# Optimization experiments

Measured on AMD Instinct MI355X. Metric: run time of the kernel, lower is better.

The kernel has to match this reference:

```python
import jax, jax.numpy as jnp
import numpy as np

H = 16          # nhead
N_LAYERS = 4    # stacks (weights are SHARED across stacks, as in the torch module)
PAD_IDX = 1
EPS = 1e-6
NEG = -1e9


def _pos_encoding(S, d):
    den = jnp.exp(-jnp.arange(0, d, 2, dtype=jnp.float32) * (np.log(10000.0) / d))
    ang = jnp.arange(S, dtype=jnp.float32)[:, None] * den[None, :]  # (S, d/2)
    pe = jnp.zeros((S, d), jnp.float32)
    pe = pe.at[:, 0::2].set(jnp.sin(ang)).at[:, 1::2].set(jnp.cos(ang))
    return pe


def _layer_norm(x, g, b):
    mu = jnp.mean(x, axis=-1, keepdims=True)
    var = jnp.mean((x - mu) ** 2, axis=-1, keepdims=True)
    return (x - mu) * jax.lax.rsqrt(var + EPS) * g + b


def _split_heads(x):
    B, S, d = x.shape
    return x.reshape(B, S, H, d // H).transpose(0, 2, 1, 3)  # (B,H,S,dk)


def _mha(q_in, k_in, v_in, mask, wq, bq, wk, bk, wv, bv, wo, bo):
    q = _split_heads(q_in @ wq + bq)
    k = _split_heads(k_in @ wk + bk)
    v = _split_heads(v_in @ wv + bv)
    dk = v.shape[-1]
    score = jnp.einsum('bhqd,bhkd->bhqk', q, k) / jnp.sqrt(jnp.float32(dk))
    if mask is not None:
        score = jnp.where(mask, score, NEG)
    p = jax.nn.softmax(score, axis=-1)
    out = jnp.einsum('bhqk,bhkd->bhqd', p, v)
    B, _, S, _ = out.shape
    out = out.transpose(0, 2, 1, 3).reshape(B, S, H * dk)
    return out @ wo + bo


def setup_inputs() -> dict:
    key = jax.random.key(0)
    B, St, Sm, d, dff, V = 4, 1024, 1024, 1024, 4096, 32000
    ks = jax.random.split(key, 32)
    sc = 1.0 / np.sqrt(d)
    inp = {
        'target_result': jax.random.randint(ks[0], (B, St), 0, V),
        'memory': jax.random.normal(ks[1], (B, Sm, d), jnp.float32),
        'emb': jax.random.normal(ks[2], (V, d), jnp.float32) * sc,
        'ff_w1': jax.random.normal(ks[3], (d, dff), jnp.float32) * sc,
        'ff_b1': jnp.zeros((dff,), jnp.float32),
        'ff_w2': jax.random.normal(ks[4], (dff, d), jnp.float32) / np.sqrt(dff),
        'ff_b2': jnp.zeros((d,), jnp.float32),
        'ln_g': jnp.ones((d,), jnp.float32),
        'ln_b': jnp.zeros((d,), jnp.float32),
    }
    i = 5
    for pre in ('sa', 'xa'):
        for nm in ('q', 'k', 'v', 'o'):
            inp[f'{pre}_w{nm}'] = jax.random.normal(ks[i], (d, d), jnp.float32) * sc
            inp[f'{pre}_b{nm}'] = jnp.zeros((d,), jnp.float32)
            i += 1
    return inp


def reference(target_result, memory, emb,
              sa_wq, sa_bq, sa_wk, sa_bk, sa_wv, sa_bv, sa_wo, sa_bo,
              xa_wq, xa_bq, xa_wk, xa_bk, xa_wv, xa_bv, xa_wo, xa_bo,
              ff_w1, ff_b1, ff_w2, ff_b2, ln_g, ln_b):
    B, St = target_result.shape
    d = emb.shape[1]
    # embed + scale + positional encoding (dropout = eval/identity)
    x = emb[target_result] * jnp.sqrt(jnp.float32(d)) + _pos_encoding(St, d)[None]
    # masks: pad mask (B,1,St,1) & causal (St,St) -> (B,1,St,St); source mask all-ones -> None
    pad = (target_result != PAD_IDX)[:, None, :, None]
    causal = jnp.tril(jnp.ones((St, St), bool))[None, None]
    tgt_mask = pad & causal
    out = x
    for _ in range(N_LAYERS):
        n = _layer_norm(out, ln_g, ln_b)
        out = out + _mha(n, n, n, tgt_mask,
                         sa_wq, sa_bq, sa_wk, sa_bk, sa_wv, sa_bv, sa_wo, sa_bo)
        n = _layer_norm(out, ln_g, ln_b)
        out = out + _mha(n, memory, memory, None,
                         xa_wq, xa_bq, xa_wk, xa_bk, xa_wv, xa_bv, xa_wo, xa_bo)
        n = _layer_norm(out, ln_g, ln_b)
        out = out + (jax.nn.relu(n @ ff_w1 + ff_b1) @ ff_w2 + ff_b2)
    return _layer_norm(out, ln_g, ln_b)
```

## Files before the change

### kernel.cpp

```cpp
#include <hip/hip_runtime.h>

typedef unsigned short u16;
typedef unsigned int u32;
typedef float f32x4 __attribute__((ext_vector_type(4)));
typedef float f32x16 __attribute__((ext_vector_type(16)));
typedef __bf16 bf16x8 __attribute__((ext_vector_type(8)));
typedef short short8 __attribute__((ext_vector_type(8)));
typedef u32 u32x4 __attribute__((ext_vector_type(4)));

#define DINLINE static __device__ __forceinline__

DINLINE u16 f2bf(float f) {
  u32 u = __builtin_bit_cast(u32, f);
  u += 0x7fffu + ((u >> 16) & 1u);
  return (u16)(u >> 16);
}

DINLINE f32x4 mfma16(short8 a, short8 b, f32x4 c) {
  return __builtin_amdgcn_mfma_f32_16x16x32_bf16(
      __builtin_bit_cast(bf16x8, a), __builtin_bit_cast(bf16x8, b), c, 0, 0, 0);
}

DINLINE f32x16 mfma32(short8 a, short8 b, f32x16 c) {
  return __builtin_amdgcn_mfma_f32_32x32x16_bf16(
      __builtin_bit_cast(bf16x8, a), __builtin_bit_cast(bf16x8, b), c, 0, 0, 0);
}

DINLINE u32 cvtpk(float lo, float hi) {
  u32 r;
  asm("v_cvt_pk_bf16_f32 %0, %1, %2" : "=v"(r) : "v"(lo), "v"(hi));
  return r;
}

DINLINE void plswap(u32& a, u32& b) {
  auto r = __builtin_amdgcn_permlane32_swap(a, b, false, false);
  a = (u32)r[0];
  b = (u32)r[1];
}

DINLINE void gld16(const void* g, void* l) {
  __builtin_amdgcn_global_load_lds(
      (const __attribute__((address_space(1))) void*)g,
      (__attribute__((address_space(3))) void*)l, 16, 0, 0);
}

__global__ __launch_bounds__(256) void transpose_wt(const float* __restrict__ src,
                                                    u16* __restrict__ dst, int K, int N,
                                                    float scale) {
  __shared__ float tile[32][33];
  int n0 = blockIdx.x * 32, k0 = blockIdx.y * 32;
  int tx = threadIdx.x, ty = threadIdx.y;
#pragma unroll
  for (int j = 0; j < 32; j += 8)
    tile[ty + j][tx] = src[(size_t)(k0 + ty + j) * N + n0 + tx];
  __syncthreads();
#pragma unroll
  for (int j = 0; j < 32; j += 8)
    dst[(size_t)(n0 + ty + j) * K + k0 + tx] = f2bf(tile[tx][ty + j] * scale);
}

__global__ __launch_bounds__(256) void cvt_bf16(const float* __restrict__ src,
                                                u16* __restrict__ dst) {
  size_t i = (size_t)blockIdx.x * 256 + threadIdx.x;
  float4 v = ((const float4*)src)[i];
  u32 lo = (u32)f2bf(v.x) | ((u32)f2bf(v.y) << 16);
  u32 hi = (u32)f2bf(v.z) | ((u32)f2bf(v.w) << 16);
  uint2 o; o.x = lo; o.y = hi;
  ((uint2*)dst)[i] = o;
}

__global__ void concat3(const float* __restrict__ a, const float* __restrict__ b,
                        const float* __restrict__ c, float* __restrict__ o, float sa) {
  int i = blockIdx.x * 256 + threadIdx.x;
  float v = (i < 1024) ? a[i] * sa : (i < 2048 ? b[i - 1024] : c[i - 2048]);
  o[i] = v;
}

__global__ void scale_vec(const float* __restrict__ a, float* __restrict__ o, float s) {
  int i = blockIdx.x * 256 + threadIdx.x;
  o[i] = a[i] * s;
}

__global__ __launch_bounds__(256) void pe_k(float* __restrict__ pe) {
  int s = blockIdx.x;
  for (int c = threadIdx.x; c < 1024; c += 256) {
    int i = c >> 1;
    float den = expf(-(float)(2 * i) * 0.0089944739960705f);
    float ang = (float)s * den;
    pe[s * 1024 + c] = (c & 1) ? cosf(ang) : sinf(ang);
  }
}

__global__ __launch_bounds__(256) void embed_pe(const int* __restrict__ tgt,
                                                const float* __restrict__ emb,
                                                const float* __restrict__ pe,
                                                float* __restrict__ x) {
  int row = blockIdx.x;
  int s = row & 1023;
  int tok = tgt[row];
  float4 e = ((const float4*)(emb + (size_t)tok * 1024))[threadIdx.x];
  float4 p = ((const float4*)(pe + (size_t)s * 1024))[threadIdx.x];
  float4 o;
  o.x = e.x * 32.0f + p.x; o.y = e.y * 32.0f + p.y;
  o.z = e.z * 32.0f + p.z; o.w = e.w * 32.0f + p.w;
  ((float4*)(x + (size_t)row * 1024))[threadIdx.x] = o;
}

template <int MODE>
__global__ __launch_bounds__(256) void ln_k(const float* __restrict__ X,
                                            const float* __restrict__ g,
                                            const float* __restrict__ bta,
                                            u16* __restrict__ obf,
                                            float* __restrict__ of) {
  int row = blockIdx.x;
  int t = threadIdx.x;
  float4 v = ((const float4*)(X + (size_t)row * 1024))[t];
  float s = v.x + v.y + v.z + v.w;
  float sq = v.x * v.x + v.y * v.y + v.z * v.z + v.w * v.w;
#pragma unroll
  for (int o = 1; o < 64; o <<= 1) {
    s += __shfl_xor(s, o);
    sq += __shfl_xor(sq, o);
  }
  __shared__ float red[8];
  int wid = t >> 6;
  if ((t & 63) == 0) { red[wid * 2] = s; red[wid * 2 + 1] = sq; }
  __syncthreads();
  s = red[0] + red[2] + red[4] + red[6];
  sq = red[1] + red[3] + red[5] + red[7];
  float mean = s * (1.0f / 1024.0f);
  float var = sq * (1.0f / 1024.0f) - mean * mean;
  float rstd = rsqrtf(var + 1e-6f);
  float4 gv = ((const float4*)g)[t];
  float4 bv = ((const float4*)bta)[t];
  float y0 = (v.x - mean) * rstd * gv.x + bv.x;
  float y1 = (v.y - mean) * rstd * gv.y + bv.y;
  float y2 = (v.z - mean) * rstd * gv.z + bv.z;
  float y3 = (v.w - mean) * rstd * gv.w + bv.w;
  if (MODE == 1) {
    float4 o4; o4.x = y0; o4.y = y1; o4.z = y2; o4.w = y3;
    ((float4*)of)[(size_t)row * 256 + t] = o4;
  } else {
    u32 lo = (u32)f2bf(y0) | ((u32)f2bf(y1) << 16);
    u32 hi = (u32)f2bf(y2) | ((u32)f2bf(y3) << 16);
    uint2 o2; o2.x = lo; o2.y = hi;
    ((uint2*)obf)[(size_t)row * 256 + t] = o2;
  }
}

__global__ __launch_bounds__(256) void vtrans(const u16* __restrict__ V, int sV,
                                              u16* __restrict__ Vt) {
  __shared__ u16 tile[32][33];
  int s0 = blockIdx.x * 32, d0 = blockIdx.y * 32, bh = blockIdx.z;
  int b = bh >> 4, h = bh & 15;
  const u16* src = V + (size_t)b * 1024 * sV + h * 64;
  int tx = threadIdx.x, ty = threadIdx.y;
#pragma unroll
  for (int j = 0; j < 32; j += 8)
    tile[ty + j][tx] = src[(size_t)(s0 + ty + j) * sV + d0 + tx];
  __syncthreads();
  u16* dst = Vt + (size_t)bh * 64 * 1024;
#pragma unroll
  for (int j = 0; j < 32; j += 8)
    dst[(size_t)(d0 + ty + j) * 1024 + s0 + tx] = tile[tx][ty + j];
}

template <int BM, int EPI>
__global__ __launch_bounds__(256) void gemm2(
    const u16* __restrict__ A, const u16* __restrict__ Bt,
    const float* __restrict__ bias, float* __restrict__ X,
    u16* __restrict__ Cbf, int N, int K) {
  constexpr int ABYT = BM * 128;
  constexpr int BBYT = 128 * 128;
  constexpr int MF = BM / 32;
  __shared__ __align__(16) char smem[2 * (ABYT + BBYT)];

  const int tid = threadIdx.x;
  const int w = tid >> 6, l = tid & 63;
  const int lg = l >> 4, lc = l & 15;
  const int m0 = blockIdx.y * BM, n0 = blockIdx.x * 128;
  const int wr = w >> 1, wc = w & 1;
  const char* Ab = (const char*)A;
  const char* Bb = (const char*)Bt;
  const size_t sA = (size_t)K * 2;

  f32x4 acc[MF][4];
  const f32x4 zv = {0.f, 0.f, 0.f, 0.f};
#pragma unroll
  for (int m = 0; m < MF; ++m)
#pragma unroll
    for (int n = 0; n < 4; ++n) acc[m][n] = zv;

  const int srow = l >> 3;
  const int scol = ((l & 7) ^ srow) << 4;

  auto stage = [&](char* bufA, char* bufB, int kt) {
    const size_t kb = (size_t)kt << 7;
#pragma unroll
    for (int i = 0; i < BM / 32; ++i) {
      const int r = i * 32 + w * 8 + srow;
      gld16(Ab + (size_t)(m0 + r) * sA + kb + scol, bufA + (i * 4 + w) * 1024 + l * 16);
    }
#pragma unroll
    for (int i = 0; i < 4; ++i) {
      const int r = i * 32 + w * 8 + srow;
      gld16(Bb + (size_t)(n0 + r) * sA + kb + scol, bufB + (i * 4 + w) * 1024 + l * 16);
    }
  };

  stage(smem, smem + ABYT, 0);
  __syncthreads();

  const int nkt = K >> 6;
  int cur = 0;
  for (int kt = 0; kt < nkt; ++kt) {
    char* As = smem + cur * (ABYT + BBYT);
    char* Bs = As + ABYT;
    if (kt + 1 < nkt) {
      char* An = smem + (cur ^ 1) * (ABYT + BBYT);
      stage(An, An + ABYT, kt + 1);
    }
#pragma unroll
    for (int ks = 0; ks < 2; ++ks) {
      short8 af[MF], bf4[4];
#pragma unroll
      for (int m = 0; m < MF; ++m) {
        int row = wr * (BM / 2) + m * 16 + lc;
        int col = (ks * 64 + (lg << 4)) ^ ((row & 7) << 4);
        af[m] = *(const short8*)(As + row * 128 + col);
      }
#pragma unroll
      for (int n = 0; n < 4; ++n) {
        int row = wc * 64 + n * 16 + lc;
        int col = (ks * 64 + (lg << 4)) ^ ((row & 7) << 4);
        bf4[n] = *(const short8*)(Bs + row * 128 + col);
      }
#pragma unroll
      for (int m = 0; m < MF; ++m)
#pragma unroll
        for (int n = 0; n < 4; ++n) acc[m][n] = mfma16(af[m], bf4[n], acc[m][n]);
    }
    __syncthreads();
    cur ^= 1;
  }

  float bv[4];
#pragma unroll
  for (int n = 0; n < 4; ++n) bv[n] = bias[n0 + wc * 64 + n * 16 + lc];

  if (EPI <= 1) {
    u16* ct = (u16*)smem;
#pragma unroll
    for (int m = 0; m < MF; ++m)
#pragma unroll
      for (int n = 0; n < 4; ++n)
#pragma unroll
        for (int r = 0; r < 4; ++r) {
          int row = wr * (BM / 2) + m * 16 + (lg << 2) + r;
          int col = wc * 64 + n * 16 + lc;
          float v = acc[m][n][r] + bv[n];
          if (EPI == 1) v = v > 0.f ? v : 0.f;
          ct[row * 136 + col] = f2bf(v);
        }
    __syncthreads();
#pragma unroll
    for (int j = 0; j < BM / 16; ++j) {
      int c = j * 256 + tid;
      int row = c >> 4, colb = (c & 15) * 8;
      *(short8*)(Cbf + (size_t)(m0 + row) * N + n0 + colb) =
          *(const short8*)(ct + row * 136 + colb);
    }
  } else {
    float* cf = (float*)smem;
#pragma unroll
    for (int m = 0; m < MF; ++m)
#pragma unroll
      for (int n = 0; n < 4; ++n)
#pragma unroll
        for (int r = 0; r < 4; ++r) {
          int row = wr * (BM / 2) + m * 16 + (lg << 2) + r;
          int col = wc * 64 + n * 16 + lc;
          cf[row * 128 + col] = acc[m][n][r] + bv[n];
        }
    __syncthreads();
#pragma unroll
    for (int j = 0; j < BM / 8; ++j) {
      int c = j * 256 + tid;
      int row = c >> 5, colb = (c & 31) * 4;
      size_t idx = (size_t)(m0 + row) * N + n0 + colb;
      float4 s = *(const float4*)(cf + row * 128 + colb);
      float4 xv = *(const float4*)(X + idx);
      xv.x += s.x; xv.y += s.y; xv.z += s.z; xv.w += s.w;
      *(float4*)(X + idx) = xv;
    }
  }
}

template <bool CAUSAL>
__global__ __launch_bounds__(256) void attn_lds(
    const u16* __restrict__ Qp, int sQ, const u16* __restrict__ Kp, int sK,
    const u16* __restrict__ Vt, const int* __restrict__ tgt,
    u16* __restrict__ Out) {
  __shared__ __align__(16) char smem[2][16384];
  const int tid = threadIdx.x;
  const int w = tid >> 6, l = tid & 63;
  const int bh = blockIdx.x & 63, sub = blockIdx.x >> 6;
  const int b = bh >> 4, h = bh & 15;
  const int lq = l & 31, hi = l >> 5;
  const int qt = sub * 4 + w;
  const int q0 = qt * 32;

  const char* Kc = (const char*)(Kp + (size_t)b * 1024 * sK + h * 64);
  const char* Vc = (const char*)(Vt + (size_t)bh * 64 * 1024);
  const u16* Qh = Qp + (size_t)b * 1024 * sQ + h * 64;

  short8 qb[4];
  {
    const u16* qrow = Qh + (size_t)(q0 + lq) * sQ + hi * 8;
#pragma unroll
    for (int c = 0; c < 4; ++c) qb[c] = *(const short8*)(qrow + c * 16);
  }

  bool row_ok = true;
  int my_nkt = 16;
  int blk_nkt = CAUSAL ? (sub * 2 + 2) : 16;
  if (CAUSAL) {
    row_ok = (tgt[b * 1024 + q0 + lq] != 1);
    bool anypad_w = __any(!row_ok);
    __shared__ int s_pad;
    if (tid == 0) s_pad = 0;
    __syncthreads();
    if (anypad_w && l == 0) s_pad = 1;
    __syncthreads();
    if (s_pad) { my_nkt = 16; blk_nkt = 16; }
    else my_nkt = (qt >> 1) + 1;
  }

  const int srow = l >> 3;
  const int scol = ((l & 7) ^ srow) << 4;
  auto stage = [&](int buf, int kt) {
    const int k0 = kt * 64;
    char* Ks = smem[buf];
    char* Vs = smem[buf] + 8192;
#pragma unroll
    for (int i = 0; i < 2; ++i) {
      const int r = i * 32 + w * 8 + srow;
      gld16(Kc + (size_t)(k0 + r) * sK * 2 + scol, Ks + r * 128);
      gld16(Vc + (size_t)r * 2048 + (size_t)k0 * 2 + scol, Vs + r * 128);
    }
  };

  float m = -3.0e38f, lsum = 0.f;
  f32x16 oacc[2];
#pragma unroll
  for (int r = 0; r < 16; ++r) { oacc[0][r] = 0.f; oacc[1][r] = 0.f; }

  stage(0, 0);
  __syncthreads();
  int cur = 0;

  for (int kt = 0; kt < blk_nkt; ++kt) {
    if (kt + 1 < blk_nkt) stage(cur ^ 1, kt + 1);
    if (kt < my_nkt) {
      const char* Ks = smem[cur];
      const char* Vs = smem[cur] + 8192;
      const int k0 = kt * 64;
      f32x16 st[2];
#pragma unroll
      for (int s = 0; s < 2; ++s) {
        const int row = s * 32 + lq;
        const int swz = (row & 7) << 4;
        f32x16 a;
#pragma unroll
        for (int r = 0; r < 16; ++r) a[r] = 0.f;
#pragma unroll
        for (int c = 0; c < 4; ++c) {
          short8 kb = *(const short8*)(Ks + row * 128 + ((c * 32 + hi * 16) ^ swz));
          a = mfma32(kb, qb[c], a);
        }
        st[s] = a;
      }
      if (CAUSAL) {
#pragma unroll
        for (int s = 0; s < 2; ++s) {
          if (!row_ok || (k0 + s * 32 + 31 > q0)) {
#pragma unroll
            for (int r = 0; r < 16; ++r) {
              int kg = k0 + s * 32 + (r & 3) + 8 * (r >> 2) + 4 * hi;
              bool ok = row_ok && (kg <= q0 + lq);
              if (!ok) st[s][r] = -1e9f;
            }
          }
        }
      }
      float tm;
      {
        float v[16];
#pragma unroll
        for (int r = 0; r < 16; ++r) v[r] = fmaxf(st[0][r], st[1][r]);
#pragma unroll
        for (int w2 = 8; w2 >= 1; w2 >>= 1)
#pragma unroll
          for (int r = 0; r < w2; ++r) v[r] = fmaxf(v[r], v[r + w2]);
        tm = v[0];
      }
      tm = fmaxf(tm, __shfl_xor(tm, 32));
      if (!__all(tm <= m + 8.0f)) {
        float mn = fmaxf(m, tm);
        float alpha = __expf(m - mn);
        lsum *= alpha;
        m = mn;
#pragma unroll
        for (int r = 0; r < 16; ++r) {
          int crow = (r & 3) + 8 * (r >> 2) + 4 * hi;
          float av = __shfl(alpha, crow);
          oacc[0][r] *= av;
          oacc[1][r] *= av;
        }
      }
      float tsa0 = 0.f, tsa1 = 0.f, tsa2 = 0.f, tsa3 = 0.f;
#pragma unroll
      for (int s = 0; s < 2; ++s) {
#pragma unroll
        for (int r = 0; r < 16; ++r) {
          float e = __expf(st[s][r] - m);
          st[s][r] = e;
          if ((r & 3) == 0) tsa0 += e;
          else if ((r & 3) == 1) tsa1 += e;
          else if ((r & 3) == 2) tsa2 += e;
          else tsa3 += e;
        }
      }
      float ts = (tsa0 + tsa1) + (tsa2 + tsa3);
      ts += __shfl_xor(ts, 32);
      lsum += ts;
      short8 pa[4];
#pragma unroll
      for (int s = 0; s < 2; ++s) {
        u32 cc[8];
#pragma unroll
        for (int t = 0; t < 4; ++t) {
          cc[2 * t]     = cvtpk(st[s][4 * t + 0], st[s][4 * t + 1]);
          cc[2 * t + 1] = cvtpk(st[s][4 * t + 2], st[s][4 * t + 3]);
        }
        plswap(cc[0], cc[2]);
        plswap(cc[1], cc[3]);
        plswap(cc[4], cc[6]);
        plswap(cc[5], cc[7]);
        u32x4 w0 = {cc[0], cc[1], cc[2], cc[3]};
        u32x4 w1 = {cc[4], cc[5], cc[6], cc[7]};
        pa[2 * s]     = __builtin_bit_cast(short8, w0);
        pa[2 * s + 1] = __builtin_bit_cast(short8, w1);
      }
#pragma unroll
      for (int dt = 0; dt < 2; ++dt) {
        const int row = dt * 32 + lq;
        const int swz = (row & 7) << 4;
#pragma unroll
        for (int c = 0; c < 4; ++c) {
          short8 vb = *(const short8*)(Vs + row * 128 + ((c * 32 + hi * 16) ^ swz));
          oacc[dt] = mfma32(pa[c], vb, oacc[dt]);
        }
      }
    }
    __syncthreads();
    cur ^= 1;
  }

#pragma unroll
  for (int r = 0; r < 16; ++r) {
    int crow = (r & 3) + 8 * (r >> 2) + 4 * hi;
    float lv = __shfl(lsum, crow);
    float linv = 1.0f / lv;
    int qg = q0 + crow;
    size_t base = ((size_t)b * 1024 + qg) * 1024 + h * 64 + lq;
    Out[base] = f2bf(oacc[0][r] * linv);
    Out[base + 32] = f2bf(oacc[1][r] * linv);
  }
}

extern "C" void kernel_launch(void* const* d_in, const int* in_sizes, int n_in,
                              void* d_out, int out_size, void* d_ws, size_t ws_size,
                              hipStream_t stream) {
  const int* tgt = (const int*)d_in[0];
  const float* memory = (const float*)d_in[1];
  const float* emb = (const float*)d_in[2];
  const float* ff_w1 = (const float*)d_in[3];
  const float* ff_b1 = (const float*)d_in[4];
  const float* ff_w2 = (const float*)d_in[5];
  const float* ff_b2 = (const float*)d_in[6];
  const float* ln_g = (const float*)d_in[7];
  const float* ln_b = (const float*)d_in[8];
  const float* sa_wq = (const float*)d_in[9];
  const float* sa_bq = (const float*)d_in[10];
  const float* sa_wk = (const float*)d_in[11];
  const float* sa_bk = (const float*)d_in[12];
  const float* sa_wv = (const float*)d_in[13];
  const float* sa_bv = (const float*)d_in[14];
  const float* sa_wo = (const float*)d_in[15];
  const float* sa_bo = (const float*)d_in[16];
  const float* xa_wq = (const float*)d_in[17];
  const float* xa_bq = (const float*)d_in[18];
  const float* xa_wk = (const float*)d_in[19];
  const float* xa_bk = (const float*)d_in[20];
  const float* xa_wv = (const float*)d_in[21];
  const float* xa_bv = (const float*)d_in[22];
  const float* xa_wo = (const float*)d_in[23];
  const float* xa_bo = (const float*)d_in[24];

  char* ws = (char*)d_ws;
  size_t off = 0;
  auto alloc = [&](size_t bytes) {
    char* p = ws + off;
    off += (bytes + 255) & ~(size_t)255;
    return p;
  };
  float* x   = (float*)alloc(4096ull * 1024 * 4);
  u16* nbf   = (u16*)alloc(4096ull * 1024 * 2);
  u16* qkv   = (u16*)alloc(4096ull * 3072 * 2);
  u16* q2    = (u16*)alloc(4096ull * 1024 * 2);
  u16* attn  = (u16*)alloc(4096ull * 1024 * 2);
  u16* vt    = (u16*)alloc(64ull * 64 * 1024 * 2);
  u16* kx    = (u16*)alloc(4096ull * 1024 * 2);
  u16* vtx   = (u16*)alloc(64ull * 64 * 1024 * 2);
  u16* h1    = (u16*)alloc(4096ull * 4096 * 2);
  u16* memb  = (u16*)alloc(4096ull * 1024 * 2);
  u16* w_qkv = (u16*)alloc(3072ull * 1024 * 2);
  u16* w_sao = (u16*)alloc(1024ull * 1024 * 2);
  u16* w_xaq = (u16*)alloc(1024ull * 1024 * 2);
  u16* w_xak = (u16*)alloc(1024ull * 1024 * 2);
  u16* w_xav = (u16*)alloc(1024ull * 1024 * 2);
  u16* w_xao = (u16*)alloc(1024ull * 1024 * 2);
  u16* w_ff1 = (u16*)alloc(4096ull * 1024 * 2);
  u16* w_ff2 = (u16*)alloc(1024ull * 4096 * 2);
  float* b_qkv = (float*)alloc(3072 * 4);
  float* b_xaq = (float*)alloc(1024 * 4);
  float* pe    = (float*)alloc(1024ull * 1024 * 4);

  dim3 blk(256);
  dim3 b32(32, 8);
  const float QS = 0.125f;

  transpose_wt<<<dim3(32, 32), b32, 0, stream>>>(sa_wq, w_qkv, 1024, 1024, QS);
  transpose_wt<<<dim3(32, 32), b32, 0, stream>>>(sa_wk, w_qkv + 1024 * 1024, 1024, 1024, 1.f);
  transpose_wt<<<dim3(32, 32), b32, 0, stream>>>(sa_wv, w_qkv + 2048 * 1024, 1024, 1024, 1.f);
  transpose_wt<<<dim3(32, 32), b32, 0, stream>>>(sa_wo, w_sao, 1024, 1024, 1.f);
  transpose_wt<<<dim3(32, 32), b32, 0, stream>>>(xa_wq, w_xaq, 1024, 1024, QS);
  transpose_wt<<<dim3(32, 32), b32, 0, stream>>>(xa_wk, w_xak, 1024, 1024, 1.f);
  transpose_wt<<<dim3(32, 32), b32, 0, stream>>>(xa_wv, w_xav, 1024, 1024, 1.f);
  transpose_wt<<<dim3(32, 32), b32, 0, stream>>>(xa_wo, w_xao, 1024, 1024, 1.f);
  transpose_wt<<<dim3(128, 32), b32, 0, stream>>>(ff_w1, w_ff1, 1024, 4096, 1.f);
  transpose_wt<<<dim3(32, 128), b32, 0, stream>>>(ff_w2, w_ff2, 4096, 1024, 1.f);
  concat3<<<12, blk, 0, stream>>>(sa_bq, sa_bk, sa_bv, b_qkv, QS);
  scale_vec<<<4, blk, 0, stream>>>(xa_bq, b_xaq, QS);
  cvt_bf16<<<4096, blk, 0, stream>>>(memory, memb);
  pe_k<<<1024, blk, 0, stream>>>(pe);
  embed_pe<<<4096, blk, 0, stream>>>(tgt, emb, pe, x);

  gemm2<64, 0><<<dim3(8, 64), blk, 0, stream>>>(memb, w_xak, xa_bk, nullptr, kx, 1024, 1024);
  gemm2<64, 0><<<dim3(8, 64), blk, 0, stream>>>(memb, w_xav, xa_bv, nullptr, attn, 1024, 1024);
  vtrans<<<dim3(32, 2, 64), b32, 0, stream>>>(attn, 1024, vtx);

  for (int layer = 0; layer < 4; ++layer) {
    ln_k<0><<<4096, blk, 0, stream>>>(x, ln_g, ln_b, nbf, nullptr);
    gemm2<128, 0><<<dim3(24, 32), blk, 0, stream>>>(nbf, w_qkv, b_qkv, nullptr, qkv, 3072, 1024);
    vtrans<<<dim3(32, 2, 64), b32, 0, stream>>>(qkv + 2048, 3072, vt);
    attn_lds<true><<<512, blk, 0, stream>>>(qkv, 3072, qkv + 1024, 3072, vt, tgt, attn);
    gemm2<64, 2><<<dim3(8, 64), blk, 0, stream>>>(attn, w_sao, sa_bo, x, nullptr, 1024, 1024);
    ln_k<0><<<4096, blk, 0, stream>>>(x, ln_g, ln_b, nbf, nullptr);
    gemm2<64, 0><<<dim3(8, 64), blk, 0, stream>>>(nbf, w_xaq, b_xaq, nullptr, q2, 1024, 1024);
    attn_lds<false><<<512, blk, 0, stream>>>(q2, 1024, kx, 1024, vtx, nullptr, attn);
    gemm2<64, 2><<<dim3(8, 64), blk, 0, stream>>>(attn, w_xao, xa_bo, x, nullptr, 1024, 1024);
    ln_k<0><<<4096, blk, 0, stream>>>(x, ln_g, ln_b, nbf, nullptr);
    gemm2<128, 1><<<dim3(32, 32), blk, 0, stream>>>(nbf, w_ff1, ff_b1, nullptr, h1, 4096, 1024);
    gemm2<64, 2><<<dim3(8, 64), blk, 0, stream>>>(h1, w_ff2, ff_b2, x, nullptr, 1024, 4096);
  }
  ln_k<1><<<4096, blk, 0, stream>>>(x, ln_g, ln_b, nullptr, (float*)d_out);
}
```

Before: 1.142 ms.

## Fuse V transpose into GEMM epilogue, bf16 residual copy, bigger attention stages, setprio

Adds a GEMM epilogue that writes V directly in the transposed per-head layout, so the separate vtrans kernels and the 3072-wide QKV output go away. The residual adds now also write a bf16 copy of x, which intermediate LayerNorms read instead of fp32, halving their read bytes but computing their statistics on rounded values. The attention kernel stages 128 keys per buffer with doubled LDS, and s_setprio is raised around the MFMA sections in both the GEMM and attention kernels. Together these aim to cut launches and memory traffic, at the cost of slight precision loss and lower attention occupancy.

```diff
diff --git a/kernel.cpp b/kernel.cpp
--- a/kernel.cpp
+++ b/kernel.cpp
@@ -14,6 +14,11 @@
   u32 u = __builtin_bit_cast(u32, f);
   u += 0x7fffu + ((u >> 16) & 1u);
   return (u16)(u >> 16);
+}
+
+DINLINE float b2f(u32 lo16) {
+  u32 u = lo16 << 16;
+  return __builtin_bit_cast(float, u);
 }
 
 DINLINE f32x4 mfma16(short8 a, short8 b, f32x4 c) {
@@ -94,7 +99,8 @@
 __global__ __launch_bounds__(256) void embed_pe(const int* __restrict__ tgt,
                                                 const float* __restrict__ emb,
                                                 const float* __restrict__ pe,
-                                                float* __restrict__ x) {
+                                                float* __restrict__ x,
+                                                u16* __restrict__ xbf) {
   int row = blockIdx.x;
   int s = row & 1023;
   int tok = tgt[row];
@@ -104,19 +110,30 @@
   o.x = e.x * 32.0f + p.x; o.y = e.y * 32.0f + p.y;
   o.z = e.z * 32.0f + p.z; o.w = e.w * 32.0f + p.w;
   ((float4*)(x + (size_t)row * 1024))[threadIdx.x] = o;
+  ushort4 ob;
+  ob.x = f2bf(o.x); ob.y = f2bf(o.y); ob.z = f2bf(o.z); ob.w = f2bf(o.w);
+  ((ushort4*)(xbf + (size_t)row * 1024))[threadIdx.x] = ob;
 }
 
 template <int MODE>
-__global__ __launch_bounds__(256) void ln_k(const float* __restrict__ X,
+__global__ __launch_bounds__(256) void ln_k(const float* __restrict__ Xf,
+                                            const u16* __restrict__ Xb,
                                             const float* __restrict__ g,
                                             const float* __restrict__ bta,
                                             u16* __restrict__ obf,
                                             float* __restrict__ of) {
   int row = blockIdx.x;
   int t = threadIdx.x;
-  float4 v = ((const float4*)(X + (size_t)row * 1024))[t];
-  float s = v.x + v.y + v.z + v.w;
-  float sq = v.x * v.x + v.y * v.y + v.z * v.z + v.w * v.w;
+  float v0, v1, v2, v3;
+  if (MODE == 1) {
+    float4 v = ((const float4*)(Xf + (size_t)row * 1024))[t];
+    v0 = v.x; v1 = v.y; v2 = v.z; v3 = v.w;
+  } else {
+    uint2 p2 = ((const uint2*)(Xb + (size_t)row * 1024))[t];
+    v0 = b2f(p2.x); v1 = b2f(p2.x >> 16); v2 = b2f(p2.y); v3 = b2f(p2.y >> 16);
+  }
+  float s = v0 + v1 + v2 + v3;
+  float sq = v0 * v0 + v1 * v1 + v2 * v2 + v3 * v3;
 #pragma unroll
   for (int o = 1; o < 64; o <<= 1) {
     s += __shfl_xor(s, o);
@@ -133,10 +150,10 @@
   float rstd = rsqrtf(var + 1e-6f);
   float4 gv = ((const float4*)g)[t];
   float4 bv = ((const float4*)bta)[t];
-  float y0 = (v.x - mean) * rstd * gv.x + bv.x;
-  float y1 = (v.y - mean) * rstd * gv.y + bv.y;
-  float y2 = (v.z - mean) * rstd * gv.z + bv.z;
-  float y3 = (v.w - mean) * rstd * gv.w + bv.w;
+  float y0 = (v0 - mean) * rstd * gv.x + bv.x;
+  float y1 = (v1 - mean) * rstd * gv.y + bv.y;
+  float y2 = (v2 - mean) * rstd * gv.z + bv.z;
+  float y3 = (v3 - mean) * rstd * gv.w + bv.w;
   if (MODE == 1) {
     float4 o4; o4.x = y0; o4.y = y1; o4.z = y2; o4.w = y3;
     ((float4*)of)[(size_t)row * 256 + t] = o4;
@@ -146,23 +163,6 @@
     uint2 o2; o2.x = lo; o2.y = hi;
     ((uint2*)obf)[(size_t)row * 256 + t] = o2;
   }
-}
-
-__global__ __launch_bounds__(256) void vtrans(const u16* __restrict__ V, int sV,
-                                              u16* __restrict__ Vt) {
-  __shared__ u16 tile[32][33];
-  int s0 = blockIdx.x * 32, d0 = blockIdx.y * 32, bh = blockIdx.z;
-  int b = bh >> 4, h = bh & 15;
-  const u16* src = V + (size_t)b * 1024 * sV + h * 64;
-  int tx = threadIdx.x, ty = threadIdx.y;
-#pragma unroll
-  for (int j = 0; j < 32; j += 8)
-    tile[ty + j][tx] = src[(size_t)(s0 + ty + j) * sV + d0 + tx];
-  __syncthreads();
-  u16* dst = Vt + (size_t)bh * 64 * 1024;
-#pragma unroll
-  for (int j = 0; j < 32; j += 8)
-    dst[(size_t)(d0 + ty + j) * 1024 + s0 + tx] = tile[tx][ty + j];
 }
 
 template <int BM, int EPI>
@@ -220,6 +220,7 @@
       char* An = smem + (cur ^ 1) * (ABYT + BBYT);
       stage(An, An + ABYT, kt + 1);
     }
+    __builtin_amdgcn_s_setprio(1);
 #pragma unroll
     for (int ks = 0; ks < 2; ++ks) {
       short8 af[MF], bf4[4];
@@ -240,6 +241,7 @@
 #pragma unroll
         for (int n = 0; n < 4; ++n) acc[m][n] = mfma16(af[m], bf4[n], acc[m][n]);
     }
+    __builtin_amdgcn_s_setprio(0);
     __syncthreads();
     cur ^= 1;
   }
@@ -270,7 +272,7 @@
       *(short8*)(Cbf + (size_t)(m0 + row) * N + n0 + colb) =
           *(const short8*)(ct + row * 136 + colb);
     }
-  } else {
+  } else if (EPI == 2) {
     float* cf = (float*)smem;
 #pragma unroll
     for (int m = 0; m < MF; ++m)
@@ -288,10 +290,36 @@
       int c = j * 256 + tid;
       int row = c >> 5, colb = (c & 31) * 4;
       size_t idx = (size_t)(m0 + row) * N + n0 + colb;
-      float4 s = *(const float4*)(cf + row * 128 + colb);
+      float4 s4 = *(const float4*)(cf + row * 128 + colb);
       float4 xv = *(const float4*)(X + idx);
-      xv.x += s.x; xv.y += s.y; xv.z += s.z; xv.w += s.w;
+      xv.x += s4.x; xv.y += s4.y; xv.z += s4.z; xv.w += s4.w;
       *(float4*)(X + idx) = xv;
+      ushort4 ob;
+      ob.x = f2bf(xv.x); ob.y = f2bf(xv.y); ob.z = f2bf(xv.z); ob.w = f2bf(xv.w);
+      *(ushort4*)(Cbf + idx) = ob;
+    }
+  } else {
+    u16* ct = (u16*)smem;
+#pragma unroll
+    for (int m = 0; m < MF; ++m)
+#pragma unroll
+      for (int n = 0; n < 4; ++n)
+#pragma unroll
+        for (int r = 0; r < 4; ++r) {
+          int row = wr * (BM / 2) + m * 16 + (lg << 2) + r;
+          int col = wc * 64 + n * 16 + lc;
+          ct[col * 136 + row] = f2bf(acc[m][n][r] + bv[n]);
+        }
+    __syncthreads();
+    const int bb = m0 >> 10, ms = m0 & 1023;
+#pragma unroll
+    for (int j = 0; j < BM / 16; ++j) {
+      int flat = j * 256 + tid;
+      int sb = flat & (BM / 8 - 1);
+      int col = flat / (BM / 8);
+      int n = n0 + col;
+      u16* dst = Cbf + (size_t)(((bb << 4) + (n >> 6)) * 64 + (n & 63)) * 1024 + ms + sb * 8;
+      *(short8*)dst = *(const short8*)(ct + col * 136 + sb * 8);
     }
   }
 }
@@ -301,7 +329,7 @@
     const u16* __restrict__ Qp, int sQ, const u16* __restrict__ Kp, int sK,
     const u16* __restrict__ Vt, const int* __restrict__ tgt,
     u16* __restrict__ Out) {
-  __shared__ __align__(16) char smem[2][16384];
+  __shared__ __align__(16) char smem[2][32768];
   const int tid = threadIdx.x;
   const int w = tid >> 6, l = tid & 63;
   const int bh = blockIdx.x & 63, sub = blockIdx.x >> 6;
@@ -323,7 +351,7 @@
 
   bool row_ok = true;
   int my_nkt = 16;
-  int blk_nkt = CAUSAL ? (sub * 2 + 2) : 16;
+  int blk_nst = CAUSAL ? (sub + 1) : 8;
   if (CAUSAL) {
     row_ok = (tgt[b * 1024 + q0 + lq] != 1);
     bool anypad_w = __any(!row_ok);
@@ -332,22 +360,25 @@
     __syncthreads();
     if (anypad_w && l == 0) s_pad = 1;
     __syncthreads();
-    if (s_pad) { my_nkt = 16; blk_nkt = 16; }
+    if (s_pad) { my_nkt = 16; blk_nst = 8; }
     else my_nkt = (qt >> 1) + 1;
   }
 
   const int srow = l >> 3;
   const int scol = ((l & 7) ^ srow) << 4;
-  auto stage = [&](int buf, int kt) {
-    const int k0 = kt * 64;
+  auto stage = [&](int buf, int st) {
+    const int k0 = st * 128;
     char* Ks = smem[buf];
-    char* Vs = smem[buf] + 8192;
-#pragma unroll
-    for (int i = 0; i < 2; ++i) {
-      const int r = i * 32 + w * 8 + srow;
-      gld16(Kc + (size_t)(k0 + r) * sK * 2 + scol, Ks + r * 128);
-      gld16(Vc + (size_t)r * 2048 + (size_t)k0 * 2 + scol, Vs + r * 128);
-    }
+    char* Vs = smem[buf] + 16384;
+#pragma unroll
+    for (int t2 = 0; t2 < 2; ++t2)
+#pragma unroll
+      for (int i = 0; i < 2; ++i) {
+        const int r = i * 32 + w * 8 + srow;
+        gld16(Kc + (size_t)(k0 + t2 * 64 + r) * sK * 2 + scol, Ks + t2 * 8192 + r * 128);
+        gld16(Vc + (size_t)r * 2048 + (size_t)(k0 + t2 * 64) * 2 + scol,
+              Vs + t2 * 8192 + r * 128);
+      }
   };
 
   float m = -3.0e38f, lsum = 0.f;
@@ -359,108 +390,116 @@
   __syncthreads();
   int cur = 0;
 
-  for (int kt = 0; kt < blk_nkt; ++kt) {
-    if (kt + 1 < blk_nkt) stage(cur ^ 1, kt + 1);
-    if (kt < my_nkt) {
-      const char* Ks = smem[cur];
-      const char* Vs = smem[cur] + 8192;
-      const int k0 = kt * 64;
-      f32x16 st[2];
-#pragma unroll
-      for (int s = 0; s < 2; ++s) {
-        const int row = s * 32 + lq;
-        const int swz = (row & 7) << 4;
-        f32x16 a;
-#pragma unroll
-        for (int r = 0; r < 16; ++r) a[r] = 0.f;
-#pragma unroll
-        for (int c = 0; c < 4; ++c) {
-          short8 kb = *(const short8*)(Ks + row * 128 + ((c * 32 + hi * 16) ^ swz));
-          a = mfma32(kb, qb[c], a);
-        }
-        st[s] = a;
-      }
-      if (CAUSAL) {
+  for (int st = 0; st < blk_nst; ++st) {
+    if (st + 1 < blk_nst) stage(cur ^ 1, st + 1);
+#pragma unroll
+    for (int t2 = 0; t2 < 2; ++t2) {
+      const int t64 = st * 2 + t2;
+      if (t64 < my_nkt) {
+        const char* Ks = smem[cur] + t2 * 8192;
+        const char* Vs = smem[cur] + 16384 + t2 * 8192;
+        const int k0 = t64 * 64;
+        f32x16 stt[2];
+        __builtin_amdgcn_s_setprio(1);
 #pragma unroll
         for (int s = 0; s < 2; ++s) {
-          if (!row_ok || (k0 + s * 32 + 31 > q0)) {
-#pragma unroll
-            for (int r = 0; r < 16; ++r) {
-              int kg = k0 + s * 32 + (r & 3) + 8 * (r >> 2) + 4 * hi;
-              bool ok = row_ok && (kg <= q0 + lq);
-              if (!ok) st[s][r] = -1e9f;
+          const int row = s * 32 + lq;
+          const int swz = (row & 7) << 4;
+          f32x16 a;
+#pragma unroll
+          for (int r = 0; r < 16; ++r) a[r] = 0.f;
+#pragma unroll
+          for (int c = 0; c < 4; ++c) {
+            short8 kb = *(const short8*)(Ks + row * 128 + ((c * 32 + hi * 16) ^ swz));
+            a = mfma32(kb, qb[c], a);
+          }
+          stt[s] = a;
+        }
+        __builtin_amdgcn_s_setprio(0);
+        if (CAUSAL) {
+#pragma unroll
+          for (int s = 0; s < 2; ++s) {
+            if (!row_ok || (k0 + s * 32 + 31 > q0)) {
+#pragma unroll
+              for (int r = 0; r < 16; ++r) {
+                int kg = k0 + s * 32 + (r & 3) + 8 * (r >> 2) + 4 * hi;
+                bool ok = row_ok && (kg <= q0 + lq);
+                if (!ok) stt[s][r] = -1e9f;
+              }
             }
           }
         }
-      }
-      float tm;
-      {
-        float v[16];
-#pragma unroll
-        for (int r = 0; r < 16; ++r) v[r] = fmaxf(st[0][r], st[1][r]);
-#pragma unroll
-        for (int w2 = 8; w2 >= 1; w2 >>= 1)
-#pragma unroll
-          for (int r = 0; r < w2; ++r) v[r] = fmaxf(v[r], v[r + w2]);
-        tm = v[0];
-      }
-      tm = fmaxf(tm, __shfl_xor(tm, 32));
-      if (!__all(tm <= m + 8.0f)) {
-        float mn = fmaxf(m, tm);
-        float alpha = __expf(m - mn);
-        lsum *= alpha;
-        m = mn;
-#pragma unroll
-        for (int r = 0; r < 16; ++r) {
-          int crow = (r & 3) + 8 * (r >> 2) + 4 * hi;
-          float av = __shfl(alpha, crow);
-          oacc[0][r] *= av;
-          oacc[1][r] *= av;
-        }
-      }
-      float tsa0 = 0.f, tsa1 = 0.f, tsa2 = 0.f, tsa3 = 0.f;
-#pragma unroll
-      for (int s = 0; s < 2; ++s) {
-#pragma unroll
-        for (int r = 0; r < 16; ++r) {
-          float e = __expf(st[s][r] - m);
-          st[s][r] = e;
-          if ((r & 3) == 0) tsa0 += e;
-          else if ((r & 3) == 1) tsa1 += e;
-          else if ((r & 3) == 2) tsa2 += e;
-          else tsa3 += e;
-        }
-      }
-      float ts = (tsa0 + tsa1) + (tsa2 + tsa3);
-      ts += __shfl_xor(ts, 32);
-      lsum += ts;
-      short8 pa[4];
-#pragma unroll
-      for (int s = 0; s < 2; ++s) {
-        u32 cc[8];
-#pragma unroll
-        for (int t = 0; t < 4; ++t) {
-          cc[2 * t]     = cvtpk(st[s][4 * t + 0], st[s][4 * t + 1]);
-          cc[2 * t + 1] = cvtpk(st[s][4 * t + 2], st[s][4 * t + 3]);
-        }
-        plswap(cc[0], cc[2]);
-        plswap(cc[1], cc[3]);
-        plswap(cc[4], cc[6]);
-        plswap(cc[5], cc[7]);
-        u32x4 w0 = {cc[0], cc[1], cc[2], cc[3]};
-        u32x4 w1 = {cc[4], cc[5], cc[6], cc[7]};
-        pa[2 * s]     = __builtin_bit_cast(short8, w0);
-        pa[2 * s + 1] = __builtin_bit_cast(short8, w1);
-      }
-#pragma unroll
-      for (int dt = 0; dt < 2; ++dt) {
-        const int row = dt * 32 + lq;
-        const int swz = (row & 7) << 4;
-#pragma unroll
-        for (int c = 0; c < 4; ++c) {
-          short8 vb = *(const short8*)(Vs + row * 128 + ((c * 32 + hi * 16) ^ swz));
-          oacc[dt] = mfma32(pa[c], vb, oacc[dt]);
-        }
+        float tm;
+        {
+          float v[16];
+#pragma unroll
+          for (int r = 0; r < 16; ++r) v[r] = fmaxf(stt[0][r], stt[1][r]);
+#pragma unroll
+          for (int w2 = 8; w2 >= 1; w2 >>= 1)
+#pragma unroll
+            for (int r = 0; r < w2; ++r) v[r] = fmaxf(v[r], v[r + w2]);
+          tm = v[0];
+        }
+        tm = fmaxf(tm, __shfl_xor(tm, 32));
+        if (!__all(tm <= m + 8.0f)) {
+          float mn = fmaxf(m, tm);
+          float alpha = __expf(m - mn);
+          lsum *= alpha;
+          m = mn;
+#pragma unroll
+          for (int r = 0; r < 16; ++r) {
+            int crow = (r & 3) + 8 * (r >> 2) + 4 * hi;
+            float av = __shfl(alpha, crow);
+            oacc[0][r] *= av;
+            oacc[1][r] *= av;
+          }
+        }
+        float tsa0 = 0.f, tsa1 = 0.f, tsa2 = 0.f, tsa3 = 0.f;
+#pragma unroll
+        for (int s = 0; s < 2; ++s) {
+#pragma unroll
+          for (int r = 0; r < 16; ++r) {
+            float e = __expf(stt[s][r] - m);
+            stt[s][r] = e;
+            if ((r & 3) == 0) tsa0 += e;
+            else if ((r & 3) == 1) tsa1 += e;
+            else if ((r & 3) == 2) tsa2 += e;
+            else tsa3 += e;
+          }
+        }
+        float ts = (tsa0 + tsa1) + (tsa2 + tsa3);
+        ts += __shfl_xor(ts, 32);
+        lsum += ts;
+        short8 pa[4];
+#pragma unroll
+        for (int s = 0; s < 2; ++s) {
+          u32 cc[8];
+#pragma unroll
+          for (int t = 0; t < 4; ++t) {
+            cc[2 * t]     = cvtpk(stt[s][4 * t + 0], stt[s][4 * t + 1]);
+            cc[2 * t + 1] = cvtpk(stt[s][4 * t + 2], stt[s][4 * t + 3]);
+          }
+          plswap(cc[0], cc[2]);
+          plswap(cc[1], cc[3]);
+          plswap(cc[4], cc[6]);
+          plswap(cc[5], cc[7]);
+          u32x4 w0 = {cc[0], cc[1], cc[2], cc[3]};
+          u32x4 w1 = {cc[4], cc[5], cc[6], cc[7]};
+          pa[2 * s]     = __builtin_bit_cast(short8, w0);
+          pa[2 * s + 1] = __builtin_bit_cast(short8, w1);
+        }
+        __builtin_amdgcn_s_setprio(1);
+#pragma unroll
+        for (int dt = 0; dt < 2; ++dt) {
+          const int row = dt * 32 + lq;
+          const int swz = (row & 7) << 4;
+#pragma unroll
+          for (int c = 0; c < 4; ++c) {
+            short8 vb = *(const short8*)(Vs + row * 128 + ((c * 32 + hi * 16) ^ swz));
+            oacc[dt] = mfma32(pa[c], vb, oacc[dt]);
+          }
+        }
+        __builtin_amdgcn_s_setprio(0);
       }
     }
     __syncthreads();
@@ -516,8 +555,9 @@
     return p;
   };
   float* x   = (float*)alloc(4096ull * 1024 * 4);
+  u16* xbf   = (u16*)alloc(4096ull * 1024 * 2);
   u16* nbf   = (u16*)alloc(4096ull * 1024 * 2);
-  u16* qkv   = (u16*)alloc(4096ull * 3072 * 2);
+  u16* qkv   = (u16*)alloc(4096ull * 2048 * 2);
   u16* q2    = (u16*)alloc(4096ull * 1024 * 2);
   u16* attn  = (u16*)alloc(4096ull * 1024 * 2);
   u16* vt    = (u16*)alloc(64ull * 64 * 1024 * 2);
@@ -555,25 +595,25 @@
   scale_vec<<<4, blk, 0, stream>>>(xa_bq, b_xaq, QS);
   cvt_bf16<<<4096, blk, 0, stream>>>(memory, memb);
   pe_k<<<1024, blk, 0, stream>>>(pe);
-  embed_pe<<<4096, blk, 0, stream>>>(tgt, emb, pe, x);
+  embed_pe<<<4096, blk, 0, stream>>>(tgt, emb, pe, x, xbf);
 
   gemm2<64, 0><<<dim3(8, 64), blk, 0, stream>>>(memb, w_xak, xa_bk, nullptr, kx, 1024, 1024);
-  gemm2<64, 0><<<dim3(8, 64), blk, 0, stream>>>(memb, w_xav, xa_bv, nullptr, attn, 1024, 1024);
-  vtrans<<<dim3(32, 2, 64), b32, 0, stream>>>(attn, 1024, vtx);
+  gemm2<64, 3><<<dim3(8, 64), blk, 0, stream>>>(memb, w_xav, xa_bv, nullptr, vtx, 1024, 1024);
 
   for (int layer = 0; layer < 4; ++layer) {
-    ln_k<0><<<4096, blk, 0, stream>>>(x, ln_g, ln_b, nbf, nullptr);
-    gemm2<128, 0><<<dim3(24, 32), blk, 0, stream>>>(nbf, w_qkv, b_qkv, nullptr, qkv, 3072, 1024);
-    vtrans<<<dim3(32, 2, 64), b32, 0, stream>>>(qkv + 2048, 3072, vt);
-    attn_lds<true><<<512, blk, 0, stream>>>(qkv, 3072, qkv + 1024, 3072, vt, tgt, attn);
-    gemm2<64, 2><<<dim3(8, 64), blk, 0, stream>>>(attn, w_sao, sa_bo, x, nullptr, 1024, 1024);
-    ln_k<0><<<4096, blk, 0, stream>>>(x, ln_g, ln_b, nbf, nullptr);
+    ln_k<2><<<4096, blk, 0, stream>>>(nullptr, xbf, ln_g, ln_b, nbf, nullptr);
+    gemm2<128, 0><<<dim3(16, 32), blk, 0, stream>>>(nbf, w_qkv, b_qkv, nullptr, qkv, 2048, 1024);
+    gemm2<64, 3><<<dim3(8, 64), blk, 0, stream>>>(nbf, w_qkv + 2048 * 1024, b_qkv + 2048,
+                                                  nullptr, vt, 1024, 1024);
+    attn_lds<true><<<512, blk, 0, stream>>>(qkv, 2048, qkv + 1024, 2048, vt, tgt, attn);
+    gemm2<64, 2><<<dim3(8, 64), blk, 0, stream>>>(attn, w_sao, sa_bo, x, xbf, 1024, 1024);
+    ln_k<2><<<4096, blk, 0, stream>>>(nullptr, xbf, ln_g, ln_b, nbf, nullptr);
     gemm2<64, 0><<<dim3(8, 64), blk, 0, stream>>>(nbf, w_xaq, b_xaq, nullptr, q2, 1024, 1024);
     attn_lds<false><<<512, blk, 0, stream>>>(q2, 1024, kx, 1024, vtx, nullptr, attn);
-    gemm2<64, 2><<<dim3(8, 64), blk, 0, stream>>>(attn, w_xao, xa_bo, x, nullptr, 1024, 1024);
-    ln_k<0><<<4096, blk, 0, stream>>>(x, ln_g, ln_b, nbf, nullptr);
+    gemm2<64, 2><<<dim3(8, 64), blk, 0, stream>>>(attn, w_xao, xa_bo, x, xbf, 1024, 1024);
+    ln_k<2><<<4096, blk, 0, stream>>>(nullptr, xbf, ln_g, ln_b, nbf, nullptr);
     gemm2<128, 1><<<dim3(32, 32), blk, 0, stream>>>(nbf, w_ff1, ff_b1, nullptr, h1, 4096, 1024);
-    gemm2<64, 2><<<dim3(8, 64), blk, 0, stream>>>(h1, w_ff2, ff_b2, x, nullptr, 1024, 4096);
-  }
-  ln_k<1><<<4096, blk, 0, stream>>>(x, ln_g, ln_b, nullptr, (float*)d_out);
-}
+    gemm2<64, 2><<<dim3(8, 64), blk, 0, stream>>>(h1, w_ff2, ff_b2, x, xbf, 1024, 4096);
+  }
+  ln_k<1><<<4096, blk, 0, stream>>>(x, nullptr, ln_g, ln_b, nullptr, (float*)d_out);
+}
```

Result: no change. 1.136 ms (-0.5%).
